# Optimization experiments

Hardware: AMD Instinct MI355X
Metric: run time of the kernel (lower is better)

The kernel has to match this reference:

```python
import jax, jax.numpy as jnp
import numpy as np

N = 50000      # cells (nodes)
E = 1600000    # directed edges (kNN connectivity graph)
F_IN = 2000    # highly-variable genes
HID = 16
H = 4          # GAT heads
C = 16         # GAT out channels per head
NUM_CLASSES = 3


def setup_inputs() -> dict:
    key = jax.random.key(0)
    ks = jax.random.split(key, 10)
    x = jax.random.normal(ks[0], (N, F_IN), dtype=jnp.float32)
    edge_index = jax.random.randint(ks[1], (2, E), 0, N, dtype=jnp.int64)
    s = 0.05
    W1 = jax.random.normal(ks[2], (F_IN, HID), dtype=jnp.float32) * s
    b1 = jnp.zeros((HID,), jnp.float32)
    Wg = jax.random.normal(ks[3], (HID, H * C), dtype=jnp.float32) * s
    att_src = jax.random.normal(ks[4], (H, C), dtype=jnp.float32) * s
    att_dst = jax.random.normal(ks[5], (H, C), dtype=jnp.float32) * s
    bg = jnp.zeros((H * C,), jnp.float32)
    Wo = jax.random.normal(ks[6], (H * C, NUM_CLASSES), dtype=jnp.float32) * s
    bo = jnp.zeros((NUM_CLASSES,), jnp.float32)
    return {"x": x, "edge_index": edge_index, "W1": W1, "b1": b1, "Wg": Wg,
            "att_src": att_src, "att_dst": att_dst, "bg": bg, "Wo": Wo, "bo": bo}


def reference(x, edge_index, W1, b1, Wg, att_src, att_dst, bg, Wo, bo):
    n = x.shape[0]
    loops = jnp.arange(n, dtype=edge_index.dtype)
    src = jnp.concatenate([edge_index[0], loops])  # [E+N]
    dst = jnp.concatenate([edge_index[1], loops])

    # ---- GCNConv(F_IN -> 16): project, symmetric-normalize, scatter-add ----
    h = x @ W1                                                   # [N, 16]
    deg = jax.ops.segment_sum(jnp.ones(src.shape, h.dtype), dst, num_segments=n)
    dinv = jnp.where(deg > 0, jax.lax.rsqrt(deg), 0.0)
    norm = dinv[src] * dinv[dst]                                 # [E+N]
    h = jax.ops.segment_sum(h[src] * norm[:, None], dst, num_segments=n) + b1
    h = jax.nn.relu(h)                                           # dropout is identity in eval

    # ---- GATConv(16 -> 16, heads=4, concat) ----
    g = (h @ Wg).reshape(n, H, C)                                # [N, H, C]
    a_s = jnp.einsum('nhc,hc->nh', g, att_src)                   # [N, H]
    a_d = jnp.einsum('nhc,hc->nh', g, att_dst)
    e = jax.nn.leaky_relu(a_s[src] + a_d[dst], 0.2)              # [E+N, H]
    m = jax.ops.segment_max(e, dst, num_segments=n)              # segment softmax (stable)
    ex = jnp.exp(e - m[dst])
    denom = jax.ops.segment_sum(ex, dst, num_segments=n)
    alpha = ex / (denom[dst] + 1e-16)                            # [E+N, H]
    out = jax.ops.segment_sum(g[src] * alpha[:, :, None], dst, num_segments=n)
    out = out.reshape(n, H * C) + bg                             # [N, 64]

    # ---- classifier head ----
    logits = out @ Wo + bo                                       # [N, 3]
    return jax.nn.log_softmax(logits, axis=1)
```

## Files before the change

kernel.cpp:

```cpp
#include <hip/hip_runtime.h>
#include <hip/hip_bf16.h>
#include <math.h>

#define F_IN   2000
#define HID    16
#define HEADS  4
#define CPH    16
#define HC     64
#define NCLS   3

__device__ __forceinline__ float lrelu(float x){ return x > 0.f ? x : 0.2f*x; }

__device__ __forceinline__ float comp4(const float4& v, int k){
  return k==0 ? v.x : k==1 ? v.y : k==2 ? v.z : v.w;
}

__device__ __forceinline__ float bf2f(unsigned short u){
  return __uint_as_float(((unsigned)u) << 16);
}

__global__ void k_zero(int* __restrict__ deg, int n) {
  int i = blockIdx.x * 256 + threadIdx.x;
  if (i < n) deg[i] = 0;
}

__global__ __launch_bounds__(256) void k_gemm1(const float* __restrict__ x,
                                               const float* __restrict__ W1,
                                               __hip_bfloat16* __restrict__ h0b,
                                               int n) {
  __shared__ float w1s[8192];
  const int t    = threadIdx.x;
  const int lane = t & 63;
  const int wid  = t >> 6;
  const int rowbase = blockIdx.x * 16 + wid * 4;

  float acc[64];
  #pragma unroll
  for (int v = 0; v < 64; ++v) acc[v] = 0.f;

  float4 sreg[8];
  float4 xs[3][4];

  auto stage_load = [&](int p) {
    const size_t kbase = (size_t)p * 500 * 16;
    #pragma unroll
    for (int b = 0; b < 8; ++b) {
      int f = t + 256 * b;
      int fc = (f < 2000) ? f : 1999;
      sreg[b] = *reinterpret_cast<const float4*>(W1 + kbase + (size_t)fc * 4);
    }
  };
  auto stage_write = [&]() {
    #pragma unroll
    for (int b = 0; b < 8; ++b) {
      int f = t + 256 * b;
      int k = f >> 2, q = f & 3;
      int qs = (q + (k >> 2)) & 3;
      float4 v = (f < 2000) ? sreg[b] : make_float4(0.f, 0.f, 0.f, 0.f);
      *reinterpret_cast<float4*>(w1s + k * 16 + qs * 4) = v;
    }
  };
  auto loadxs = [&](float4* xv, int ci) {
    const int f4l = (ci & 1) * 64 + lane;
    const bool kv = (f4l < 125);
    const int base = (ci >> 1) * 500 + f4l * 4;
    #pragma unroll
    for (int r = 0; r < 4; ++r) {
      xv[r] = kv ? *reinterpret_cast<const float4*>(x + (size_t)(rowbase + r) * F_IN + base)
                 : make_float4(0.f, 0.f, 0.f, 0.f);
    }
  };
  auto compute = [&](const float4* xv, int ci) {
    const int f4l = (ci & 1) * 64 + lane;
    #pragma unroll
    for (int kk = 0; kk < 4; ++kk) {
      const int rs = 4 * f4l + kk;
      const float* rowp = w1s + rs * 16;
      float xk0 = comp4(xv[0], kk), xk1 = comp4(xv[1], kk);
      float xk2 = comp4(xv[2], kk), xk3 = comp4(xv[3], kk);
      #pragma unroll
      for (int q = 0; q < 4; ++q) {
        const int qs = (q + f4l) & 3;
        float4 w4 = *reinterpret_cast<const float4*>(rowp + (qs << 2));
        acc[0*16+4*q+0] += xk0 * w4.x; acc[0*16+4*q+1] += xk0 * w4.y;
        acc[0*16+4*q+2] += xk0 * w4.z; acc[0*16+4*q+3] += xk0 * w4.w;
        acc[1*16+4*q+0] += xk1 * w4.x; acc[1*16+4*q+1] += xk1 * w4.y;
        acc[1*16+4*q+2] += xk1 * w4.z; acc[1*16+4*q+3] += xk1 * w4.w;
        acc[2*16+4*q+0] += xk2 * w4.x; acc[2*16+4*q+1] += xk2 * w4.y;
        acc[2*16+4*q+2] += xk2 * w4.z; acc[2*16+4*q+3] += xk2 * w4.w;
        acc[3*16+4*q+0] += xk3 * w4.x; acc[3*16+4*q+1] += xk3 * w4.y;
        acc[3*16+4*q+2] += xk3 * w4.z; acc[3*16+4*q+3] += xk3 * w4.w;
      }
    }
  };

  stage_load(0);
  loadxs(xs[0], 0);
  loadxs(xs[1], 1);
  stage_write();
  __syncthreads();

  #pragma unroll
  for (int ci = 0; ci < 8; ++ci) {
    if ((ci & 1) == 0 && ci < 6) stage_load((ci >> 1) + 1);
    if (ci < 6) loadxs(xs[(ci + 2) % 3], ci + 2);
    compute(xs[ci % 3], ci);
    if ((ci & 1) == 1 && ci < 7) {
      __syncthreads();
      stage_write();
      __syncthreads();
    }
  }

  #pragma unroll
  for (int b = 32; b >= 1; b >>= 1) {
    bool hi = (lane & b) != 0;
    #pragma unroll
    for (int j = 0; j < b; ++j) {
      float send = hi ? acc[j] : acc[b + j];
      float recv = __shfl_xor(send, b);
      acc[j] = (hi ? acc[b + j] : acc[j]) + recv;
    }
  }
  int r = lane >> 4, c = lane & 15;
  int row = rowbase + r;
  if (row < n) h0b[(size_t)row * 16 + c] = __float2bfloat16(acc[0]);
}

__global__ void k_deg(const int* __restrict__ edst, int* __restrict__ deg, int e) {
  int i = blockIdx.x * 256 + threadIdx.x;
  if (i < e) atomicAdd(&deg[edst[i]], 1);
}

__global__ void k_scan_a(const int* __restrict__ deg, int* __restrict__ bsum, int n) {
  __shared__ int s[256];
  int i = blockIdx.x * 256 + threadIdx.x;
  s[threadIdx.x] = (i < n) ? deg[i] : 0;
  __syncthreads();
  for (int off = 128; off > 0; off >>= 1) {
    if (threadIdx.x < off) s[threadIdx.x] += s[threadIdx.x + off];
    __syncthreads();
  }
  if (threadIdx.x == 0) bsum[blockIdx.x] = s[0];
}

__global__ void k_scan_b(int* __restrict__ bsum, int nb) {
  int lane = threadIdx.x;
  int carry = 0;
  for (int base = 0; base < nb; base += 64) {
    int idx = base + lane;
    int orig = (idx < nb) ? bsum[idx] : 0;
    int v = orig;
    #pragma unroll
    for (int off = 1; off < 64; off <<= 1) {
      int tv = __shfl_up(v, off);
      if (lane >= off) v += tv;
    }
    if (idx < nb) bsum[idx] = carry + v - orig;
    carry += __shfl(v, 63);
  }
}

__global__ void k_scan_c(const int* __restrict__ deg, const int* __restrict__ bsum,
                         int* __restrict__ rowptr, int* __restrict__ cursor,
                         float* __restrict__ dinv, int n) {
  __shared__ int s[256];
  int i = blockIdx.x * 256 + threadIdx.x;
  int v = (i < n) ? deg[i] : 0;
  s[threadIdx.x] = v;
  __syncthreads();
  for (int off = 1; off < 256; off <<= 1) {
    int tv = (threadIdx.x >= off) ? s[threadIdx.x - off] : 0;
    __syncthreads();
    s[threadIdx.x] += tv;
    __syncthreads();
  }
  int excl = s[threadIdx.x] - v + bsum[blockIdx.x];
  if (i < n) {
    rowptr[i] = excl;
    cursor[i] = excl;
    dinv[i] = rsqrtf((float)(v + 1));
    if (i == n - 1) rowptr[n] = excl + v;
  }
}

__global__ void k_scatter(const int* __restrict__ esrc, const int* __restrict__ edst,
                          int* __restrict__ cursor, int* __restrict__ csr, int e) {
  int i = blockIdx.x * 256 + threadIdx.x;
  if (i < e) {
    int d = edst[i];
    int pos = atomicAdd(&cursor[d], 1);
    csr[pos] = esrc[i];
  }
}

__global__ __launch_bounds__(256) void k_gcn(
    const unsigned short* __restrict__ h0b, const int* __restrict__ rowptr,
    const int* __restrict__ csr, const float* __restrict__ dinv,
    const float* __restrict__ b1, const float* __restrict__ Wg,
    const float* __restrict__ atts, const float* __restrict__ attd,
    __hip_bfloat16* __restrict__ gb, float* __restrict__ a_s,
    float* __restrict__ a_d, int n) {
  __shared__ float wgs[HID * HC];
  __shared__ float ats[HC], atd[HC];
  int t = threadIdx.x;
  for (int i = t; i < HID * HC; i += 256) wgs[i] = Wg[i];
  if (t < HC) { ats[t] = atts[t]; atd[t] = attd[t]; }
  __syncthreads();

  int lane = t & 63, w = t >> 6;
  int dst = blockIdx.x * 4 + w;
  if (dst >= n) return;
  int j = lane >> 4, c = lane & 15;
  int start = rowptr[dst], end = rowptr[dst + 1];
  float dd = dinv[dst];

  float acc = 0.f;
  for (int idx = start + j; idx < end; idx += 4) {
    int src = csr[idx];
    acc += bf2f(h0b[(size_t)src * 16 + c]) * dinv[src];
  }
  acc += __shfl_xor(acc, 16);
  acc += __shfl_xor(acc, 32);
  acc = acc * dd + bf2f(h0b[(size_t)dst * 16 + c]) * dd * dd;
  float hv = fmaxf(acc + b1[c], 0.f);

  float go = 0.f;
  #pragma unroll
  for (int k = 0; k < 16; ++k) {
    float hk = __shfl(hv, k);
    go += hk * wgs[k * HC + lane];
  }
  gb[(size_t)dst * HC + lane] = __float2bfloat16(go);

  float asv = go * ats[lane], adv = go * atd[lane];
  #pragma unroll
  for (int m = 1; m < 16; m <<= 1) {
    asv += __shfl_xor(asv, m);
    adv += __shfl_xor(adv, m);
  }
  if (c == 0) {
    a_s[(size_t)dst * 4 + j] = asv;
    a_d[(size_t)dst * 4 + j] = adv;
  }
}

__global__ __launch_bounds__(256) void k_gat(
    const unsigned short* __restrict__ gb, const int* __restrict__ rowptr,
    const int* __restrict__ csr, const float* __restrict__ a_s,
    const float* __restrict__ a_d, const float* __restrict__ bg,
    const float* __restrict__ Wo, const float* __restrict__ bo,
    float* __restrict__ out, int n) {
  __shared__ float wos[HC * NCLS];
  __shared__ float bgs[HC];
  __shared__ float bos[NCLS];
  int t = threadIdx.x;
  if (t < HC * NCLS) wos[t] = Wo[t];
  if (t < HC) bgs[t] = bg[t];
  if (t < NCLS) bos[t] = bo[t];
  __syncthreads();

  int lane = t & 63, w = t >> 6;
  int dst = blockIdx.x * 4 + w;
  if (dst >= n) return;
  int start = rowptr[dst], end = rowptr[dst + 1];
  int j = lane >> 4, c = lane & 15, h = c >> 2;

  float adh = a_d[(size_t)dst * 4 + h];
  float ash = a_s[(size_t)dst * 4 + h];

  float m = -1e30f, den = 0.f;
  float a0 = 0.f, a1 = 0.f, a2 = 0.f, a3 = 0.f;

  for (int idx = start + j; idx < end; idx += 4) {
    int src = csr[idx];
    float e = lrelu(a_s[(size_t)src * 4 + h] + adh);
    float mn = fmaxf(m, e);
    float corr = __expf(m - mn);
    float p = __expf(e - mn);
    ushort4 u4 = *reinterpret_cast<const ushort4*>(gb + (size_t)src * HC + c * 4);
    den = den * corr + p;
    a0 = a0 * corr + p * bf2f(u4.x);
    a1 = a1 * corr + p * bf2f(u4.y);
    a2 = a2 * corr + p * bf2f(u4.z);
    a3 = a3 * corr + p * bf2f(u4.w);
    m = mn;
  }
  if (j == 0) {
    float e = lrelu(ash + adh);
    float mn = fmaxf(m, e);
    float corr = __expf(m - mn);
    float p = __expf(e - mn);
    ushort4 u4 = *reinterpret_cast<const ushort4*>(gb + (size_t)dst * HC + c * 4);
    den = den * corr + p;
    a0 = a0 * corr + p * bf2f(u4.x);
    a1 = a1 * corr + p * bf2f(u4.y);
    a2 = a2 * corr + p * bf2f(u4.z);
    a3 = a3 * corr + p * bf2f(u4.w);
    m = mn;
  }

  #pragma unroll
  for (int msk = 16; msk <= 32; msk <<= 1) {
    float m2 = __shfl_xor(m, msk);
    float d2 = __shfl_xor(den, msk);
    float b0 = __shfl_xor(a0, msk);
    float b1v = __shfl_xor(a1, msk);
    float b2 = __shfl_xor(a2, msk);
    float b3 = __shfl_xor(a3, msk);
    float M = fmaxf(m, m2);
    float c1 = __expf(m - M), c2 = __expf(m2 - M);
    den = den * c1 + d2 * c2;
    a0 = a0 * c1 + b0 * c2;
    a1 = a1 * c1 + b1v * c2;
    a2 = a2 * c1 + b2 * c2;
    a3 = a3 * c1 + b3 * c2;
    m = M;
  }
  den += 1e-16f;

  float o0 = a0 / den + bgs[c * 4 + 0];
  float o1 = a1 / den + bgs[c * 4 + 1];
  float o2 = a2 / den + bgs[c * 4 + 2];
  float o3 = a3 / den + bgs[c * 4 + 3];

  float p0 = 0.f, p1 = 0.f, p2 = 0.f;
  {
    int ch = c * 4;
    p0 += o0 * wos[(ch+0)*NCLS+0] + o1 * wos[(ch+1)*NCLS+0] + o2 * wos[(ch+2)*NCLS+0] + o3 * wos[(ch+3)*NCLS+0];
    p1 += o0 * wos[(ch+0)*NCLS+1] + o1 * wos[(ch+1)*NCLS+1] + o2 * wos[(ch+2)*NCLS+1] + o3 * wos[(ch+3)*NCLS+1];
    p2 += o0 * wos[(ch+0)*NCLS+2] + o1 * wos[(ch+1)*NCLS+2] + o2 * wos[(ch+2)*NCLS+2] + o3 * wos[(ch+3)*NCLS+2];
  }
  #pragma unroll
  for (int msk = 1; msk < 16; msk <<= 1) {
    p0 += __shfl_xor(p0, msk);
    p1 += __shfl_xor(p1, msk);
    p2 += __shfl_xor(p2, msk);
  }
  p0 += bos[0]; p1 += bos[1]; p2 += bos[2];
  float mx = fmaxf(p0, fmaxf(p1, p2));
  float ls = mx + logf(__expf(p0 - mx) + __expf(p1 - mx) + __expf(p2 - mx));
  if (lane == 0) {
    out[(size_t)dst * 3 + 0] = p0 - ls;
    out[(size_t)dst * 3 + 1] = p1 - ls;
    out[(size_t)dst * 3 + 2] = p2 - ls;
  }
}

extern "C" void kernel_launch(void* const* d_in, const int* in_sizes, int n_in,
                              void* d_out, int out_size, void* d_ws, size_t ws_size,
                              hipStream_t stream) {
  const float* x    = (const float*)d_in[0];
  const int*   ei   = (const int*)  d_in[1];
  const float* W1   = (const float*)d_in[2];
  const float* b1   = (const float*)d_in[3];
  const float* Wg   = (const float*)d_in[4];
  const float* atts = (const float*)d_in[5];
  const float* attd = (const float*)d_in[6];
  const float* bg   = (const float*)d_in[7];
  const float* Wo   = (const float*)d_in[8];
  const float* bo   = (const float*)d_in[9];
  float* out = (float*)d_out;

  const int n = in_sizes[0] / F_IN;
  const int e = in_sizes[1] / 2;
  const int* esrc = ei;
  const int* edst = ei + e;

  char* p = (char*)d_ws;
  auto alloc = [&](size_t bytes) { char* r = p; p += (bytes + 255) & ~(size_t)255; return r; };
  __hip_bfloat16* h0b = (__hip_bfloat16*)alloc((size_t)n * 16 * 2);
  int*   deg    = (int*)  alloc((size_t)n * 4);
  int*   cursor = (int*)  alloc((size_t)n * 4);
  float* dinv   = (float*)alloc((size_t)n * 4);
  int*   rowptr = (int*)  alloc((size_t)(n + 1) * 4);
  int*   bsum   = (int*)  alloc(4096);
  int*   csr    = (int*)  alloc((size_t)e * 4);
  __hip_bfloat16* gbuf = (__hip_bfloat16*)alloc((size_t)n * HC * 2);
  float* as_    = (float*)alloc((size_t)n * 4 * 4);
  float* ad_    = (float*)alloc((size_t)n * 4 * 4);

  int nzb = (n + 255) / 256;
  k_zero<<<nzb, 256, 0, stream>>>(deg, n);

  k_gemm1<<<(n + 15) / 16, 256, 0, stream>>>(x, W1, h0b, n);

  k_deg<<<(e + 255) / 256, 256, 0, stream>>>(edst, deg, e);

  int nb = (n + 255) / 256;
  k_scan_a<<<nb, 256, 0, stream>>>(deg, bsum, n);
  k_scan_b<<<1, 64, 0, stream>>>(bsum, nb);
  k_scan_c<<<nb, 256, 0, stream>>>(deg, bsum, rowptr, cursor, dinv, n);

  k_scatter<<<(e + 255) / 256, 256, 0, stream>>>(esrc, edst, cursor, csr, e);

  k_gcn<<<(n + 3) / 4, 256, 0, stream>>>((const unsigned short*)h0b, rowptr, csr,
                                         dinv, b1, Wg, atts, attd,
                                         gbuf, as_, ad_, n);

  k_gat<<<(n + 3) / 4, 256, 0, stream>>>((const unsigned short*)gbuf, rowptr, csr,
                                         as_, ad_, bg, Wo, bo, out, n);
}
```

Measured before the change: 490.5 us.

## Fuse degree counting into GEMM kernel and stage W1 via direct global-to-LDS loads

Merges the degree-atomic kernel into the first-layer GEMM launch as extra blocks so both run concurrently in one grid. It also replaces the register-staged, software-pipelined W1 and x loading with a simpler per-phase loop that fills shared memory through global_load_lds and an XOR swizzle, and reads x directly each phase. This removes one launch and lets the atomic-heavy degree work overlap the bandwidth-bound GEMM, but it gives up the prefetch overlap of x loads with compute, which may expose memory latency.

Result: faster. 437.2 us (-10.9%).

```diff
diff --git a/kernel.cpp b/kernel.cpp
--- a/kernel.cpp
+++ b/kernel.cpp
@@ -24,11 +24,18 @@
   if (i < n) deg[i] = 0;
 }
 
-__global__ __launch_bounds__(256) void k_gemm1(const float* __restrict__ x,
-                                               const float* __restrict__ W1,
-                                               __hip_bfloat16* __restrict__ h0b,
-                                               int n) {
+__global__ __launch_bounds__(256) void k_gemm_deg(const float* __restrict__ x,
+                                                  const float* __restrict__ W1,
+                                                  __hip_bfloat16* __restrict__ h0b,
+                                                  int n, int ngemm,
+                                                  const int* __restrict__ edst,
+                                                  int* __restrict__ deg, int e) {
   __shared__ float w1s[8192];
+  if ((int)blockIdx.x >= ngemm) {
+    int i = (blockIdx.x - ngemm) * 256 + threadIdx.x;
+    if (i < e) atomicAdd(&deg[edst[i]], 1);
+    return;
+  }
   const int t    = threadIdx.x;
   const int lane = t & 63;
   const int wid  = t >> 6;
@@ -38,77 +45,60 @@
   #pragma unroll
   for (int v = 0; v < 64; ++v) acc[v] = 0.f;
 
-  float4 sreg[8];
-  float4 xs[3][4];
-
-  auto stage_load = [&](int p) {
-    const size_t kbase = (size_t)p * 500 * 16;
+  for (int phase = 0; phase < 4; ++phase) {
+    const int kbase = phase * 500;
+    __syncthreads();
     #pragma unroll
-    for (int b = 0; b < 8; ++b) {
-      int f = t + 256 * b;
-      int fc = (f < 2000) ? f : 1999;
-      sreg[b] = *reinterpret_cast<const float4*>(W1 + kbase + (size_t)fc * 4);
+    for (int k = 0; k < 8; ++k) {
+      const int slotbase = (wid * 8 + k) * 64;
+      const int slot = slotbase + lane;
+      const int row_slot = slot >> 2;
+      const int r = row_slot ^ ((row_slot >> 4) & 1);
+      const int q = (slot & 3) ^ ((row_slot >> 2) & 3);
+      int rg = kbase + r;
+      if (rg > 1999) rg = 1999;
+      __builtin_amdgcn_global_load_lds(
+          (const __attribute__((address_space(1))) void*)(W1 + (size_t)rg * 16 + q * 4),
+          (__attribute__((address_space(3))) void*)(w1s + (size_t)slotbase * 4),
+          16, 0, 0);
     }
-  };
-  auto stage_write = [&]() {
+    __syncthreads();
+
     #pragma unroll
-    for (int b = 0; b < 8; ++b) {
-      int f = t + 256 * b;
-      int k = f >> 2, q = f & 3;
-      int qs = (q + (k >> 2)) & 3;
-      float4 v = (f < 2000) ? sreg[b] : make_float4(0.f, 0.f, 0.f, 0.f);
-      *reinterpret_cast<float4*>(w1s + k * 16 + qs * 4) = v;
-    }
-  };
-  auto loadxs = [&](float4* xv, int ci) {
-    const int f4l = (ci & 1) * 64 + lane;
-    const bool kv = (f4l < 125);
-    const int base = (ci >> 1) * 500 + f4l * 4;
-    #pragma unroll
-    for (int r = 0; r < 4; ++r) {
-      xv[r] = kv ? *reinterpret_cast<const float4*>(x + (size_t)(rowbase + r) * F_IN + base)
-                 : make_float4(0.f, 0.f, 0.f, 0.f);
-    }
-  };
-  auto compute = [&](const float4* xv, int ci) {
-    const int f4l = (ci & 1) * 64 + lane;
-    #pragma unroll
-    for (int kk = 0; kk < 4; ++kk) {
-      const int rs = 4 * f4l + kk;
-      const float* rowp = w1s + rs * 16;
-      float xk0 = comp4(xv[0], kk), xk1 = comp4(xv[1], kk);
-      float xk2 = comp4(xv[2], kk), xk3 = comp4(xv[3], kk);
-      #pragma unroll
-      for (int q = 0; q < 4; ++q) {
-        const int qs = (q + f4l) & 3;
-        float4 w4 = *reinterpret_cast<const float4*>(rowp + (qs << 2));
-        acc[0*16+4*q+0] += xk0 * w4.x; acc[0*16+4*q+1] += xk0 * w4.y;
-        acc[0*16+4*q+2] += xk0 * w4.z; acc[0*16+4*q+3] += xk0 * w4.w;
-        acc[1*16+4*q+0] += xk1 * w4.x; acc[1*16+4*q+1] += xk1 * w4.y;
-        acc[1*16+4*q+2] += xk1 * w4.z; acc[1*16+4*q+3] += xk1 * w4.w;
-        acc[2*16+4*q+0] += xk2 * w4.x; acc[2*16+4*q+1] += xk2 * w4.y;
-        acc[2*16+4*q+2] += xk2 * w4.z; acc[2*16+4*q+3] += xk2 * w4.w;
-        acc[3*16+4*q+0] += xk3 * w4.x; acc[3*16+4*q+1] += xk3 * w4.y;
-        acc[3*16+4*q+2] += xk3 * w4.z; acc[3*16+4*q+3] += xk3 * w4.w;
+    for (int i = 0; i < 2; ++i) {
+      int f4l = i * 64 + lane;
+      if (f4l < 125) {
+        float4 xv[4];
+        #pragma unroll
+        for (int r = 0; r < 4; ++r) {
+          int row = rowbase + r;
+          xv[r] = (row < n)
+              ? *reinterpret_cast<const float4*>(
+                    x + (size_t)row * F_IN + kbase + f4l * 4)
+              : make_float4(0.f, 0.f, 0.f, 0.f);
+        }
+        const int qx = f4l & 3;
+        const int xb = (f4l >> 2) & 1;
+        #pragma unroll
+        for (int kk = 0; kk < 4; ++kk) {
+          const int rs = (4 * f4l + kk) ^ xb;
+          const float* rowp = w1s + rs * 16;
+          float xk0 = comp4(xv[0], kk), xk1 = comp4(xv[1], kk);
+          float xk2 = comp4(xv[2], kk), xk3 = comp4(xv[3], kk);
+          #pragma unroll
+          for (int q = 0; q < 4; ++q) {
+            float4 w4 = *reinterpret_cast<const float4*>(rowp + ((q ^ qx) << 2));
+            acc[0*16+4*q+0] += xk0 * w4.x; acc[0*16+4*q+1] += xk0 * w4.y;
+            acc[0*16+4*q+2] += xk0 * w4.z; acc[0*16+4*q+3] += xk0 * w4.w;
+            acc[1*16+4*q+0] += xk1 * w4.x; acc[1*16+4*q+1] += xk1 * w4.y;
+            acc[1*16+4*q+2] += xk1 * w4.z; acc[1*16+4*q+3] += xk1 * w4.w;
+            acc[2*16+4*q+0] += xk2 * w4.x; acc[2*16+4*q+1] += xk2 * w4.y;
+            acc[2*16+4*q+2] += xk2 * w4.z; acc[2*16+4*q+3] += xk2 * w4.w;
+            acc[3*16+4*q+0] += xk3 * w4.x; acc[3*16+4*q+1] += xk3 * w4.y;
+            acc[3*16+4*q+2] += xk3 * w4.z; acc[3*16+4*q+3] += xk3 * w4.w;
+          }
+        }
       }
-    }
-  };
-
-  stage_load(0);
-  loadxs(xs[0], 0);
-  loadxs(xs[1], 1);
-  stage_write();
-  __syncthreads();
-
-  #pragma unroll
-  for (int ci = 0; ci < 8; ++ci) {
-    if ((ci & 1) == 0 && ci < 6) stage_load((ci >> 1) + 1);
-    if (ci < 6) loadxs(xs[(ci + 2) % 3], ci + 2);
-    compute(xs[ci % 3], ci);
-    if ((ci & 1) == 1 && ci < 7) {
-      __syncthreads();
-      stage_write();
-      __syncthreads();
     }
   }
 
@@ -125,11 +115,6 @@
   int r = lane >> 4, c = lane & 15;
   int row = rowbase + r;
   if (row < n) h0b[(size_t)row * 16 + c] = __float2bfloat16(acc[0]);
-}
-
-__global__ void k_deg(const int* __restrict__ edst, int* __restrict__ deg, int e) {
-  int i = blockIdx.x * 256 + threadIdx.x;
-  if (i < e) atomicAdd(&deg[edst[i]], 1);
 }
 
 __global__ void k_scan_a(const int* __restrict__ deg, int* __restrict__ bsum, int n) {
@@ -383,9 +368,9 @@
   int nzb = (n + 255) / 256;
   k_zero<<<nzb, 256, 0, stream>>>(deg, n);
 
-  k_gemm1<<<(n + 15) / 16, 256, 0, stream>>>(x, W1, h0b, n);
-
-  k_deg<<<(e + 255) / 256, 256, 0, stream>>>(edst, deg, e);
+  const int ngemm = (n + 15) / 16;
+  const int ndeg  = (e + 255) / 256;
+  k_gemm_deg<<<ngemm + ndeg, 256, 0, stream>>>(x, W1, h0b, n, ngemm, edst, deg, e);
 
   int nb = (n + 255) / 256;
   k_scan_a<<<nb, 256, 0, stream>>>(deg, bsum, n);
```
